# Kernel optimization log

Hardware: AMD Instinct MI355X
Metric: run time of the kernel (lower is better)

## Reference

```python
import jax, jax.numpy as jnp
import numpy as np

NEG_INF = -1e30


def setup_inputs() -> dict:
    key = jax.random.key(0)
    k1, k2 = jax.random.split(key)
    B, S, H, D = 2, 2048, 16, 64
    qkv = jax.random.normal(k1, (B, S, 3, H, D), dtype=jnp.float32)
    pos_bias = jax.random.normal(k2, (H, S, S), dtype=jnp.float32)
    return {"qkv": qkv, "pos_bias": pos_bias}


def reference(qkv, pos_bias):
    # qkv: (B, S, 3, H, D); fixed-length path of FlashAttention.forward
    # (key_padding_mask=None, cu_seqlens=None) -> standard per-batch attention
    # with additive per-head positional bias and causal masking.
    B, S, _, H, D = qkv.shape
    q = qkv[:, :, 0]  # (B, S, H, D)
    k = qkv[:, :, 1]
    v = qkv[:, :, 2]
    softmax_scale = 1.0 / jnp.sqrt(jnp.asarray(D, dtype=qkv.dtype))
    # scores: (B, H, S, S)
    scores = jnp.einsum('bshd,bthd->bhst', q, k) * softmax_scale
    scores = scores + pos_bias[None]  # broadcast bias over batch
    # causal mask (query s attends to keys t <= s)
    causal = jnp.tril(jnp.ones((S, S), dtype=bool))
    scores = jnp.where(causal[None, None], scores, NEG_INF)
    attn = jax.nn.softmax(scores, axis=-1)
    # output: (B, S, H, D)
    out = jnp.einsum('bhst,bthd->bshd', attn, v)
    return out
```

## Files before the change

### kernel.cpp

```cpp
#include <hip/hip_runtime.h>

typedef float f32x4 __attribute__((ext_vector_type(4)));
typedef __bf16 bf16x8 __attribute__((ext_vector_type(8)));

#define MFMA16(a, b, c) __builtin_amdgcn_mfma_f32_16x16x32_bf16(a, b, c, 0, 0, 0)

constexpr int S = 2048, H = 16, Dh = 64;
constexpr int BR = 64, BC = 64;
#define NEG_INF_F (-1e30f)

__device__ __forceinline__ void gld16(const __bf16* g, __bf16* l) {
    __builtin_amdgcn_global_load_lds(
        (const __attribute__((address_space(1))) void*)(g),
        (__attribute__((address_space(3))) void*)(l), 16, 0, 0);
}

__global__ __launch_bounds__(256) void prep(const float* __restrict__ qkv,
                                            __bf16* __restrict__ khat,
                                            __bf16* __restrict__ vT)
{
    __shared__ __bf16 vtile[64][72];
    const int tid = threadIdx.x;
    const int bid = blockIdx.x;
    const int tt  = bid & 31;
    const int bh  = bid >> 5;
    const int b   = bh >> 4, h = bh & 15;
    const int t0  = tt * 64;
    const int tr  = tid >> 2, c0 = (tid & 3) * 16;

    const float* kp = qkv + (((size_t)(b * S + t0 + tr) * 3 + 1) * H + h) * Dh + c0;
    const float* vp = qkv + (((size_t)(b * S + t0 + tr) * 3 + 2) * H + h) * Dh + c0;
    f32x4 k0 = *(const f32x4*)(kp + 0), k1 = *(const f32x4*)(kp + 4),
          k2 = *(const f32x4*)(kp + 8), k3 = *(const f32x4*)(kp + 12);
    f32x4 v0 = *(const f32x4*)(vp + 0), v1 = *(const f32x4*)(vp + 4),
          v2 = *(const f32x4*)(vp + 8), v3 = *(const f32x4*)(vp + 12);
    bf16x8 ka, kb, va, vb;
#pragma unroll
    for (int j = 0; j < 4; ++j) {
        ka[j] = (__bf16)k0[j]; ka[4 + j] = (__bf16)k1[j];
        kb[j] = (__bf16)k2[j]; kb[4 + j] = (__bf16)k3[j];
        va[j] = (__bf16)v0[j]; va[4 + j] = (__bf16)v1[j];
        vb[j] = (__bf16)v2[j]; vb[4 + j] = (__bf16)v3[j];
    }
    {
        __bf16* kd = khat + ((size_t)bh * S + t0 + tr) * Dh;
        const int g0 = c0 >> 3, sw = tr & 7;
        *(bf16x8*)(kd + ((( g0    ) ^ sw) << 3)) = ka;
        *(bf16x8*)(kd + (((g0 + 1) ^ sw) << 3)) = kb;
    }
    *(bf16x8*)&vtile[tr][c0]     = va;
    *(bf16x8*)&vtile[tr][c0 + 8] = vb;
    __syncthreads();
    const int d = tid >> 2, tc0 = (tid & 3) * 16;
    bf16x8 x, y;
#pragma unroll
    for (int i = 0; i < 8; ++i) {
        x[i] = vtile[tc0 + i][d];
        y[i] = vtile[tc0 + 8 + i][d];
    }
    __bf16* vd = vT + ((size_t)bh * Dh + d) * S + t0;
    const int h0 = tc0 >> 3, sv = d & 7;
    *(bf16x8*)(vd + ((( h0    ) ^ sv) << 3)) = x;
    *(bf16x8*)(vd + (((h0 + 1) ^ sv) << 3)) = y;
}

__global__ __launch_bounds__(256, 4) void fa_fwd(
    const float* __restrict__ qkv, const float* __restrict__ pb,
    const __bf16* __restrict__ khat, const __bf16* __restrict__ vT,
    float* __restrict__ out)
{
    __shared__ __bf16 klds[64 * 64];
    __shared__ __bf16 vlds[2][64 * 64];
    __shared__ __bf16 plds[4][16][72];

    const int tid  = threadIdx.x;
    const int wave = tid >> 6;
    const int lane = tid & 63;
    const int quad = lane >> 4;
    const int l16  = lane & 15;

    const int g  = blockIdx.x >> 8;
    const int pp = blockIdx.x & 255;
    const int kk = pp >> 5, hb = pp & 31;
    const int b  = hb & 1, h = hb >> 1;
    const int qt = (g == 0) ? 31 - kk : (g == 1) ? 16 + kk : (g == 2) ? 15 - kk : kk;
    const int q0 = qt * BR;
    const int bh = b * H + h;
    const float scale = 0.125f;

    const int qrow = q0 + wave * 16 + l16;
    const float* qp = qkv + (((size_t)(b * S + qrow) * 3 + 0) * H + h) * Dh;
    bf16x8 qfrag[2];
#pragma unroll
    for (int ks = 0; ks < 2; ++ks) {
        f32x4 a = *(const f32x4*)(qp + ks * 32 + quad * 8);
        f32x4 c = *(const f32x4*)(qp + ks * 32 + quad * 8 + 4);
#pragma unroll
        for (int j = 0; j < 4; ++j) qfrag[ks][j] = (__bf16)a[j];
#pragma unroll
        for (int j = 0; j < 4; ++j) qfrag[ks][4 + j] = (__bf16)c[j];
    }

    const int lrow  = wave * 16 + quad * 4;
    const int myrow = q0 + lrow;
    float l_r[4] = {0.f, 0.f, 0.f, 0.f};
    f32x4 oacc[4];
#pragma unroll
    for (int dt = 0; dt < 4; ++dt) oacc[dt] = (f32x4){0.f, 0.f, 0.f, 0.f};

    const int seg = wave * 2;
    const int lt  = lane >> 3, le = (lane & 7) * 8;
    const __bf16* kg = khat + ((size_t)bh * S + (seg * 8 + lt)) * 64 + le;
    const __bf16* vg = vT   + ((size_t)bh * Dh + seg * 8 + lt) * S + le;
    __bf16* kl = klds + seg * 512;
    const int vo = seg * 512;

    const float* bb = pb + (size_t)h * S * S + (size_t)myrow * S + l16;
    const int swz = l16 & 7;

    gld16(kg,         kl);
    gld16(kg + 512,   kl + 512);
    gld16(vg,         vlds[0] + vo);
    gld16(vg + 8 * S, vlds[0] + vo + 512);
    kg += BC * 64; vg += BC;

    float bnext[16];
#pragma unroll
    for (int ct = 0; ct < 4; ++ct)
#pragma unroll
        for (int r = 0; r < 4; ++r) bnext[ct * 4 + r] = bb[(size_t)r * S + ct * 16];
    bb += BC;

    for (int it = 0; it <= qt; ++it) {
        const int cur = it & 1;
        __syncthreads();

        f32x4 sacc[4];
#pragma unroll
        for (int ct = 0; ct < 4; ++ct) sacc[ct] = (f32x4){0.f, 0.f, 0.f, 0.f};
        __builtin_amdgcn_s_setprio(1);
#pragma unroll
        for (int ct = 0; ct < 4; ++ct) {
#pragma unroll
            for (int ks = 0; ks < 2; ++ks) {
                bf16x8 kf = *(const bf16x8*)&klds[(ct * 16 + l16) * 64 + (((ks * 4 + quad) ^ swz) << 3)];
                sacc[ct] = MFMA16(qfrag[ks], kf, sacc[ct]);
            }
        }
        __builtin_amdgcn_s_setprio(0);

        __syncthreads();

        if (it < qt) {
            gld16(kg,         kl);
            gld16(kg + 512,   kl + 512);
            __bf16* vl = &vlds[cur ^ 1][vo];
            gld16(vg,         vl);
            gld16(vg + 8 * S, vl + 512);
            kg += BC * 64; vg += BC;
        }

        const bool diag = (it == qt);
#pragma unroll
        for (int ct = 0; ct < 4; ++ct) {
            const int colrel = ct * 16 + l16;
#pragma unroll
            for (int r = 0; r < 4; ++r) {
                float s = fmaf(sacc[ct][r], scale, bnext[ct * 4 + r]);
                if (diag && (colrel > lrow + r)) s = NEG_INF_F;
                float p = __expf(s);
                l_r[r] += p;
                plds[wave][quad * 4 + r][colrel] = (__bf16)p;
            }
            if (it < qt) {
#pragma unroll
                for (int r = 0; r < 4; ++r)
                    bnext[ct * 4 + r] = bb[(size_t)r * S + ct * 16];
            }
        }
        if (it < qt) bb += BC;

        bf16x8 pf[2];
#pragma unroll
        for (int ks = 0; ks < 2; ++ks)
            pf[ks] = *(const bf16x8*)&plds[wave][l16][ks * 32 + quad * 8];
        __builtin_amdgcn_s_setprio(1);
#pragma unroll
        for (int dt = 0; dt < 4; ++dt) {
#pragma unroll
            for (int ks = 0; ks < 2; ++ks) {
                bf16x8 vf = *(const bf16x8*)&vlds[cur][(dt * 16 + l16) * 64 + (((ks * 4 + quad) ^ swz) << 3)];
                oacc[dt] = MFMA16(pf[ks], vf, oacc[dt]);
            }
        }
        __builtin_amdgcn_s_setprio(0);
    }

#pragma unroll
    for (int r = 0; r < 4; ++r) {
#pragma unroll
        for (int m = 1; m < 16; m <<= 1) l_r[r] += __shfl_xor(l_r[r], m, 64);
        const float inv = 1.0f / l_r[r];
        float* op = out + (((size_t)(b * S + (myrow + r)) * H) + h) * Dh;
#pragma unroll
        for (int dt = 0; dt < 4; ++dt)
            op[dt * 16 + l16] = oacc[dt][r] * inv;
    }
}

extern "C" void kernel_launch(void* const* d_in, const int* in_sizes, int n_in,
                              void* d_out, int out_size, void* d_ws, size_t ws_size,
                              hipStream_t stream) {
    const float* qkv = (const float*)d_in[0];
    const float* pb  = (const float*)d_in[1];
    float* out       = (float*)d_out;

    constexpr size_t KV_ELEMS = (size_t)2 * H * S * Dh;
    __bf16* khat = (__bf16*)d_ws;
    __bf16* vT   = khat + KV_ELEMS;

    prep<<<dim3(1024), dim3(256), 0, stream>>>(qkv, khat, vT);
    fa_fwd<<<dim3(1024), dim3(256), 0, stream>>>(qkv, pb, khat, vT, out);
}
```

Baseline: 399.1 us.

## Transpose MFMA operands so P stays in registers and bias loads vectorize

```diff
diff --git a/kernel.cpp b/kernel.cpp
--- a/kernel.cpp
+++ b/kernel.cpp
@@ -2,6 +2,7 @@
 
 typedef float f32x4 __attribute__((ext_vector_type(4)));
 typedef __bf16 bf16x8 __attribute__((ext_vector_type(8)));
+typedef unsigned int u32x4 __attribute__((ext_vector_type(4)));
 
 #define MFMA16(a, b, c) __builtin_amdgcn_mfma_f32_16x16x32_bf16(a, b, c, 0, 0, 0)
 
@@ -71,7 +72,6 @@
 {
     __shared__ __bf16 klds[64 * 64];
     __shared__ __bf16 vlds[2][64 * 64];
-    __shared__ __bf16 plds[4][16][72];
 
     const int tid  = threadIdx.x;
     const int wave = tid >> 6;
@@ -82,7 +82,7 @@
     const int g  = blockIdx.x >> 8;
     const int pp = blockIdx.x & 255;
     const int kk = pp >> 5, hb = pp & 31;
-    const int b  = hb & 1, h = hb >> 1;
+    const int h  = hb & 15, b = hb >> 4;
     const int qt = (g == 0) ? 31 - kk : (g == 1) ? 16 + kk : (g == 2) ? 15 - kk : kk;
     const int q0 = qt * BR;
     const int bh = b * H + h;
@@ -101,9 +101,7 @@
         for (int j = 0; j < 4; ++j) qfrag[ks][4 + j] = (__bf16)c[j];
     }
 
-    const int lrow  = wave * 16 + quad * 4;
-    const int myrow = q0 + lrow;
-    float l_r[4] = {0.f, 0.f, 0.f, 0.f};
+    float lsum = 0.f;
     f32x4 oacc[4];
 #pragma unroll
     for (int dt = 0; dt < 4; ++dt) oacc[dt] = (f32x4){0.f, 0.f, 0.f, 0.f};
@@ -115,8 +113,12 @@
     __bf16* kl = klds + seg * 512;
     const int vo = seg * 512;
 
-    const float* bb = pb + (size_t)h * S * S + (size_t)myrow * S + l16;
-    const int swz = l16 & 7;
+    const float* bb = pb + (size_t)h * S * S + (size_t)qrow * S + quad * 4;
+
+    const int swz  = l16 & 7;
+    const int idxA = l16 + ((quad & 1) << 5);
+    const int idxB = idxA + 16;
+    const bool qhi = (quad >= 2);
 
     gld16(kg,         kl);
     gld16(kg + 512,   kl + 512);
@@ -124,11 +126,9 @@
     gld16(vg + 8 * S, vlds[0] + vo + 512);
     kg += BC * 64; vg += BC;
 
-    float bnext[16];
-#pragma unroll
-    for (int ct = 0; ct < 4; ++ct)
-#pragma unroll
-        for (int r = 0; r < 4; ++r) bnext[ct * 4 + r] = bb[(size_t)r * S + ct * 16];
+    f32x4 bn[4];
+#pragma unroll
+    for (int ct = 0; ct < 4; ++ct) bn[ct] = *(const f32x4*)(bb + ct * 16);
     bb += BC;
 
     for (int it = 0; it <= qt; ++it) {
@@ -144,7 +144,7 @@
 #pragma unroll
             for (int ks = 0; ks < 2; ++ks) {
                 bf16x8 kf = *(const bf16x8*)&klds[(ct * 16 + l16) * 64 + (((ks * 4 + quad) ^ swz) << 3)];
-                sacc[ct] = MFMA16(qfrag[ks], kf, sacc[ct]);
+                sacc[ct] = MFMA16(kf, qfrag[ks], sacc[ct]);
             }
         }
         __builtin_amdgcn_s_setprio(0);
@@ -161,50 +161,62 @@
         }
 
         const bool diag = (it == qt);
+        unsigned int pk[4][2];
 #pragma unroll
         for (int ct = 0; ct < 4; ++ct) {
-            const int colrel = ct * 16 + l16;
+            const f32x4 bia = bn[ct];
+            float p[4];
 #pragma unroll
             for (int r = 0; r < 4; ++r) {
-                float s = fmaf(sacc[ct][r], scale, bnext[ct * 4 + r]);
-                if (diag && (colrel > lrow + r)) s = NEG_INF_F;
-                float p = __expf(s);
-                l_r[r] += p;
-                plds[wave][quad * 4 + r][colrel] = (__bf16)p;
+                float s = fmaf(sacc[ct][r], scale, bia[r]);
+                if (diag && (ct * 16 + quad * 4 + r > wave * 16 + l16)) s = NEG_INF_F;
+                p[r] = __expf(s);
+                lsum += p[r];
             }
-            if (it < qt) {
-#pragma unroll
-                for (int r = 0; r < 4; ++r)
-                    bnext[ct * 4 + r] = bb[(size_t)r * S + ct * 16];
-            }
+            asm("v_cvt_pk_bf16_f32 %0, %1, %2" : "=v"(pk[ct][0]) : "v"(p[0]), "v"(p[1]));
+            asm("v_cvt_pk_bf16_f32 %0, %1, %2" : "=v"(pk[ct][1]) : "v"(p[2]), "v"(p[3]));
+            if (it < qt) bn[ct] = *(const f32x4*)(bb + ct * 16);
         }
         if (it < qt) bb += BC;
 
         bf16x8 pf[2];
 #pragma unroll
-        for (int ks = 0; ks < 2; ++ks)
-            pf[ks] = *(const bf16x8*)&plds[wave][l16][ks * 32 + quad * 8];
+        for (int ks = 0; ks < 2; ++ks) {
+            const int e0 = (int)pk[2 * ks][0],     e1 = (int)pk[2 * ks][1];
+            const int o0 = (int)pk[2 * ks + 1][0], o1 = (int)pk[2 * ks + 1][1];
+            const int ae0 = __shfl(e0, idxA, 64), ao0 = __shfl(o0, idxA, 64);
+            const int ae1 = __shfl(e1, idxA, 64), ao1 = __shfl(o1, idxA, 64);
+            const int be0 = __shfl(e0, idxB, 64), bo0 = __shfl(o0, idxB, 64);
+            const int be1 = __shfl(e1, idxB, 64), bo1 = __shfl(o1, idxB, 64);
+            u32x4 w;
+            w[0] = (unsigned int)(qhi ? ao0 : ae0);
+            w[1] = (unsigned int)(qhi ? ao1 : ae1);
+            w[2] = (unsigned int)(qhi ? bo0 : be0);
+            w[3] = (unsigned int)(qhi ? bo1 : be1);
+            pf[ks] = __builtin_bit_cast(bf16x8, w);
+        }
+
         __builtin_amdgcn_s_setprio(1);
 #pragma unroll
         for (int dt = 0; dt < 4; ++dt) {
 #pragma unroll
             for (int ks = 0; ks < 2; ++ks) {
                 bf16x8 vf = *(const bf16x8*)&vlds[cur][(dt * 16 + l16) * 64 + (((ks * 4 + quad) ^ swz) << 3)];
-                oacc[dt] = MFMA16(pf[ks], vf, oacc[dt]);
+                oacc[dt] = MFMA16(vf, pf[ks], oacc[dt]);
             }
         }
         __builtin_amdgcn_s_setprio(0);
     }
 
-#pragma unroll
-    for (int r = 0; r < 4; ++r) {
-#pragma unroll
-        for (int m = 1; m < 16; m <<= 1) l_r[r] += __shfl_xor(l_r[r], m, 64);
-        const float inv = 1.0f / l_r[r];
-        float* op = out + (((size_t)(b * S + (myrow + r)) * H) + h) * Dh;
-#pragma unroll
-        for (int dt = 0; dt < 4; ++dt)
-            op[dt * 16 + l16] = oacc[dt][r] * inv;
+    lsum += __shfl_xor(lsum, 16, 64);
+    lsum += __shfl_xor(lsum, 32, 64);
+    const float inv = 1.0f / lsum;
+    float* op = out + (((size_t)(b * S + qrow) * H) + h) * Dh;
+#pragma unroll
+    for (int dt = 0; dt < 4; ++dt) {
+        f32x4 r = oacc[dt];
+        r[0] *= inv; r[1] *= inv; r[2] *= inv; r[3] *= inv;
+        *(f32x4*)(op + dt * 16 + quad * 4) = r;
     }
 }
 
```

New measurement: 400.3 us. No clear change (+0.3%).
